# Optimization experiments

Hardware: AMD Instinct MI355X
Metric: run time of the kernel (lower is better)

Reference implementation:

```python
import jax, jax.numpy as jnp
import numpy as np

SQRT_2 = 1.414213
RT = 1.0  # Disk sets self.rt = 1.0
N_KPTS = 8192
M_KPTS = 8192
F_DIM = 256  # SuperPoint descriptor dim


def setup_inputs() -> dict:
    key = jax.random.key(0)
    k0, k1, k2, k3 = jax.random.split(key, 4)
    d0 = jax.random.normal(k0, (1, F_DIM, N_KPTS), dtype=jnp.float32)
    d1 = jax.random.normal(k1, (1, F_DIM, M_KPTS), dtype=jnp.float32)
    # distance_matrix assumes L2-normalized descriptors (normalize over F axis)
    d0 = d0 / jnp.linalg.norm(d0, axis=1, keepdims=True)
    d1 = d1 / jnp.linalg.norm(d1, axis=1, keepdims=True)
    kpts0 = jax.random.uniform(k2, (1, N_KPTS, 2), dtype=jnp.float32) * 480.0
    kpts1 = jax.random.uniform(k3, (1, M_KPTS, 2), dtype=jnp.float32) * 480.0
    return {"descriptors0": d0, "descriptors1": d1,
            "keypoints0": kpts0, "keypoints1": kpts1}


def _ratio_nn(dist):
    """Per-row nearest neighbor + Lowe ratio test. dist: [A, B].
    Returns (nn_idx [A] int32, pass_mask [A] bool)."""
    neg2, idx2 = jax.lax.top_k(-dist, 2)  # two smallest distances per row
    d1, d2 = -neg2[:, 0], -neg2[:, 1]
    return idx2[:, 0], (d1 / d2) < RT


def reference(descriptors0, descriptors1, keypoints0, keypoints1):
    fs0 = descriptors0[0].T  # [N, F]
    fs1 = descriptors1[0].T  # [M, F]
    # cosine -> L2-on-unit-sphere distance matrix, clamped as in the source
    dist = SQRT_2 * jnp.sqrt(jnp.clip(1.0 - fs0 @ fs1.T, 1e-6, None))  # [N, M]

    fwd_nn, fwd_ok = _ratio_nn(dist)    # [N]
    bck_nn, bck_ok = _ratio_nn(dist.T)  # [M]

    # mutual NN: (i, fwd_nn[i]) is kept iff the backward pass produced the
    # flipped pair (i, fwd_nn[i]) too -> same as counts==2 in the torch merge
    n = fs0.shape[0]
    mutual = fwd_ok & bck_ok[fwd_nn] & (bck_nn[fwd_nn] == jnp.arange(n))

    indices0 = jnp.where(mutual, fwd_nn, -1)[None, :].astype(jnp.int32)  # [1, N]
    mscores0 = jnp.where(indices0 > 0, 1, 0).astype(jnp.int32)           # [1, N]
    matches1 = jnp.full(keypoints1.shape[:-1], -1, dtype=jnp.int32)      # [1, M]
    mscores1 = jnp.zeros(keypoints1.shape[:-1], dtype=keypoints1.dtype)  # [1, M]
    return indices0, matches1, mscores0, mscores1
```

## Files before the change

kernel.cpp:

```cpp
#include <hip/hip_runtime.h>
#include <float.h>

#define NPTS 8192
#define MPTS 8192
#define FDIM 256

#define BM 128
#define BN 128
#define BK 32
#define TCT (MPTS / BN)
#define TRT (NPTS / BM)

typedef unsigned short ushort_t;
typedef unsigned int u32;
typedef __attribute__((ext_vector_type(8))) short short8;
typedef __attribute__((ext_vector_type(4))) float floatx4;

struct T2 { float s1, s2; int i1; };

__device__ __forceinline__ T2 t2_sent() { T2 a; a.s1 = -FLT_MAX; a.s2 = -FLT_MAX; a.i1 = 0; return a; }

__device__ __forceinline__ T2 t2_merge(T2 a, T2 b) {
    T2 r;
    r.s1 = fmaxf(a.s1, b.s1);
    r.i1 = (b.s1 > a.s1) ? b.i1 : a.i1;
    r.s2 = fmaxf(fminf(a.s1, b.s1), fmaxf(a.s2, b.s2));
    return r;
}
__device__ __forceinline__ T2 t2_make4(float v0, float v1, float v2, float v3,
                                       int i0, int i1_, int i2, int i3) {
    float lo01 = fminf(v0, v1), hi01 = fmaxf(v0, v1);
    float lo23 = fminf(v2, v3), hi23 = fmaxf(v2, v3);
    int a01 = (v1 > v0) ? i1_ : i0;
    int a23 = (v3 > v2) ? i3 : i2;
    T2 r;
    r.s1 = fmaxf(hi01, hi23);
    r.i1 = (hi23 > hi01) ? a23 : a01;
    r.s2 = fmaxf(fminf(hi01, hi23), fmaxf(lo01, lo23));
    return r;
}
__device__ __forceinline__ float4 t2_pack(T2 a) {
    return make_float4(a.s1, a.s2, __int_as_float(a.i1), 0.0f);
}
__device__ __forceinline__ T2 t2_unpack(float4 v) {
    T2 a; a.s1 = v.x; a.s2 = v.y; a.i1 = __float_as_int(v.z); return a;
}
__device__ __forceinline__ T2 t2_shfl_xor(T2 a, int m) {
    T2 r; r.s1 = __shfl_xor(a.s1, m); r.s2 = __shfl_xor(a.s2, m); r.i1 = __shfl_xor(a.i1, m);
    return r;
}

__device__ __forceinline__ float bf2f(ushort_t u) {
    union { u32 i; float f; } v; v.i = ((u32)u) << 16; return v.f;
}
__device__ __forceinline__ ushort_t f2bf_rtne(float x) {
    u32 u = __float_as_uint(x);
    u32 r = u + 0x7FFFu + ((u >> 16) & 1u);
    return (ushort_t)(r >> 16);
}

__global__ __launch_bounds__(256) void transpose_split(
    const float* __restrict__ s0, const float* __restrict__ s1,
    ushort_t* __restrict__ hi0, ushort_t* __restrict__ lo0,
    ushort_t* __restrict__ hi1, ushort_t* __restrict__ lo1)
{
    __shared__ ushort_t hiS[64][66];
    __shared__ ushort_t loS[64][66];
    const float* src = blockIdx.z ? s1 : s0;
    ushort_t* hiT = blockIdx.z ? hi1 : hi0;
    ushort_t* loT = blockIdx.z ? lo1 : lo0;
    const int t = threadIdx.x;
    const int n0 = blockIdx.x * 64, f0 = blockIdx.y * 64;

#pragma unroll
    for (int p = 0; p < 4; p++) {
        int fl = (t >> 4) + p * 16;
        int nl = (t & 15) * 4;
        float4 x = *(const float4*)&src[(size_t)(f0 + fl) * NPTS + n0 + nl];
        float xs[4] = {x.x, x.y, x.z, x.w};
#pragma unroll
        for (int e = 0; e < 4; e++) {
            ushort_t hb = f2bf_rtne(xs[e]);
            ushort_t lb = f2bf_rtne(xs[e] - bf2f(hb));
            hiS[nl + e][fl] = hb;
            loS[nl + e][fl] = lb;
        }
    }
    __syncthreads();
#pragma unroll
    for (int p = 0; p < 8; p++) {
        int nl = (t >> 5) + p * 8;
        int fp = (t & 31) * 2;
        u32 hw = (u32)hiS[nl][fp] | ((u32)hiS[nl][fp + 1] << 16);
        u32 lw = (u32)loS[nl][fp] | ((u32)loS[nl][fp + 1] << 16);
        size_t o = (size_t)(n0 + nl) * FDIM + f0 + fp;
        *(u32*)&hiT[o] = hw;
        *(u32*)&loT[o] = lw;
    }
}

#define GLDS(g, l) __builtin_amdgcn_global_load_lds( \
    (const __attribute__((address_space(1))) void*)(g), \
    (__attribute__((address_space(3))) void*)(l), 16, 0, 0)

#define STAGE(k0v, bufp) do { \
    _Pragma("unroll") for (int cc = 0; cc < 2; cc++) { \
        int _so = srcOff[cc] + (k0v); \
        char* _lb = (bufp) + ldsOff[cc]; \
        GLDS(bAh + _so, _lb); \
        GLDS(bBh + _so, _lb + 8192); \
        GLDS(bAl + _so, _lb + 16384); \
        GLDS(bBl + _so, _lb + 24576); \
    } \
} while (0)

#define READ_ALL(Pb) do { \
    _Pragma("unroll") for (int i = 0; i < 4; i++) { \
        ah[i] = *(const short8*)((Pb) + aoff[i]); \
        al[i] = *(const short8*)((Pb) + 16384 + aoff[i]); \
        bh[i] = *(const short8*)((Pb) + 8192 + boff[i]); \
        bl[i] = *(const short8*)((Pb) + 24576 + boff[i]); \
    } \
} while (0)

#define MFMA48 do { \
    _Pragma("unroll") for (int i = 0; i < 4; i++) \
    _Pragma("unroll") for (int j = 0; j < 4; j++) { \
        acc[i][j] = __builtin_amdgcn_mfma_f32_16x16x32_bf16(ah[i], bh[j], acc[i][j], 0, 0, 0); \
        acc[i][j] = __builtin_amdgcn_mfma_f32_16x16x32_bf16(ah[i], bl[j], acc[i][j], 0, 0, 0); \
        acc[i][j] = __builtin_amdgcn_mfma_f32_16x16x32_bf16(al[i], bh[j], acc[i][j], 0, 0, 0); \
    } \
} while (0)

#define KSTEP(ksv, Pb, Qb) do { \
    STAGE(((ksv) + 1) * BK, Qb); \
    asm volatile("s_waitcnt vmcnt(8)" ::: "memory"); \
    __builtin_amdgcn_s_barrier(); \
    READ_ALL(Pb); \
    asm volatile("s_waitcnt lgkmcnt(0)" ::: "memory"); \
    __builtin_amdgcn_sched_barrier(0); \
    MFMA48; \
    __builtin_amdgcn_sched_barrier(0); \
    __builtin_amdgcn_s_barrier(); \
} while (0)

__global__ __launch_bounds__(256, 2) void gemm_top2(
    const ushort_t* __restrict__ hiA, const ushort_t* __restrict__ loA,
    const ushort_t* __restrict__ hiB, const ushort_t* __restrict__ loB,
    float4* __restrict__ rowPart, float4* __restrict__ colPart)
{
    __shared__ char smem[65536];
    float* scrS1 = (float*)smem;
    float* scrS2 = (float*)(smem + 8448);
    int*   scrI  = (int*)(smem + 16896);
    float4* redC = (float4*)(smem + 25600);

    const int t = threadIdx.x;
    const int lane = t & 63, lc = lane & 15, q = lane >> 4;
    const int w = t >> 6, wx = w & 1, wy = w >> 1;
    const int ctile = blockIdx.x, rtile = blockIdx.y;
    const int n0 = rtile * BM, m0 = ctile * BN;

    floatx4 acc[4][4];
#pragma unroll
    for (int i = 0; i < 4; i++)
#pragma unroll
        for (int j = 0; j < 4; j++) acc[i][j] = (floatx4)0.0f;

    int srcOff[2], ldsOff[2];
#pragma unroll
    for (int cc = 0; cc < 2; cc++) {
        int L = cc * 256 + t;
        int row = L >> 2;
        int g = (L & 3) ^ ((L >> 3) & 3);
        srcOff[cc] = row * FDIM + g * 8;
        ldsOff[cc] = L * 16;
    }
    const ushort_t* bAh = hiA + (size_t)n0 * FDIM;
    const ushort_t* bAl = loA + (size_t)n0 * FDIM;
    const ushort_t* bBh = hiB + (size_t)m0 * FDIM;
    const ushort_t* bBl = loB + (size_t)m0 * FDIM;

    const int xa = (q ^ ((lc >> 1) & 3)) * 16;
    int aoff[4], boff[4];
#pragma unroll
    for (int i = 0; i < 4; i++) {
        aoff[i] = (wy * 64 + i * 16 + lc) * 64 + xa;
        boff[i] = (wx * 64 + i * 16 + lc) * 64 + xa;
    }

    short8 ah[4], al[4], bh[4], bl[4];

    char* buf0 = smem;
    char* buf1 = smem + 32768;
    STAGE(0, buf0);
#pragma unroll 1
    for (int kp = 0; kp < 3; kp++) {
        KSTEP(2 * kp, buf0, buf1);
        KSTEP(2 * kp + 1, buf1, buf0);
    }
    KSTEP(6, buf0, buf1);
    {
        asm volatile("s_waitcnt vmcnt(0)" ::: "memory");
        __builtin_amdgcn_s_barrier();
        READ_ALL(buf1);
        asm volatile("s_waitcnt lgkmcnt(0)" ::: "memory");
        __builtin_amdgcn_sched_barrier(0);
        MFMA48;
    }
    __syncthreads();

    T2 colT[4];
#pragma unroll
    for (int j = 0; j < 4; j++) colT[j] = t2_sent();
    T2 rowT[4][4];

    const int cb = m0 + wx * 64 + lc;
#pragma unroll
    for (int i = 0; i < 4; i++) {
#pragma unroll
        for (int r = 0; r < 4; r++)
            rowT[i][r] = t2_make4(acc[i][0][r], acc[i][1][r], acc[i][2][r], acc[i][3][r],
                                  cb, cb + 16, cb + 32, cb + 48);
        const int rb = n0 + wy * 64 + i * 16 + q * 4;
#pragma unroll
        for (int j = 0; j < 4; j++)
            colT[j] = t2_merge(colT[j],
                t2_make4(acc[i][j][0], acc[i][j][1], acc[i][j][2], acc[i][j][3],
                         rb, rb + 1, rb + 2, rb + 3));
    }

#pragma unroll
    for (int j = 0; j < 4; j++) {
        colT[j] = t2_merge(colT[j], t2_shfl_xor(colT[j], 16));
        colT[j] = t2_merge(colT[j], t2_shfl_xor(colT[j], 32));
        if (q == 0) redC[(wx * 64 + j * 16 + lc) * 2 + wy] = t2_pack(colT[j]);
    }

#pragma unroll
    for (int round = 0; round < 2; round++) {
        __syncthreads();
        if (wy == round) {
#pragma unroll
            for (int i = 0; i < 4; i++)
#pragma unroll
                for (int r = 0; r < 4; r++) {
                    int row = i * 16 + q * 4 + r;
                    int col = (lc << 1) | wx;
                    int slot = row * 33 + ((col + row + 9 * q) & 31);
                    scrS1[slot] = rowT[i][r].s1;
                    scrS2[slot] = rowT[i][r].s2;
                    scrI[slot]  = rowT[i][r].i1;
                }
        }
        __syncthreads();
        {
            int row = t >> 2, chunk = t & 3;
            T2 a = t2_sent();
#pragma unroll
            for (int s = 0; s < 8; s++) {
                int slot = row * 33 + ((chunk << 3) | s);
                T2 b; b.s1 = scrS1[slot]; b.s2 = scrS2[slot]; b.i1 = scrI[slot];
                a = t2_merge(a, b);
            }
            a = t2_merge(a, t2_shfl_xor(a, 1));
            a = t2_merge(a, t2_shfl_xor(a, 2));
            if (chunk == 0)
                rowPart[(size_t)ctile * NPTS + n0 + round * 64 + row] = t2_pack(a);
        }
    }

    __syncthreads();
    if (t < 128) {
        T2 m = t2_unpack(redC[t * 2 + 0]);
        m = t2_merge(m, t2_unpack(redC[t * 2 + 1]));
        colPart[(size_t)rtile * MPTS + m0 + t] = t2_pack(m);
    }
}

__global__ __launch_bounds__(256) void reduce_final(
    const float4* __restrict__ rowPart, const float4* __restrict__ colPart,
    float* __restrict__ out)
{
    __shared__ float4 sh[4][64];
    __shared__ int shFwd[64];
    __shared__ int shOk[64];
    const int t = threadIdx.x, nl = t & 63, sub = t >> 6;
    const int n = blockIdx.x * 64 + nl;

    T2 a = t2_sent();
#pragma unroll
    for (int k = 0; k < 16; k++)
        a = t2_merge(a, t2_unpack(rowPart[(size_t)(sub * 16 + k) * NPTS + n]));
    sh[sub][nl] = t2_pack(a);
    __syncthreads();
    if (t < 64) {
        T2 r = t2_unpack(sh[0][t]);
        r = t2_merge(r, t2_unpack(sh[1][t]));
        r = t2_merge(r, t2_unpack(sh[2][t]));
        r = t2_merge(r, t2_unpack(sh[3][t]));
        float c1 = fmaxf(1.0f - r.s1, 1e-6f), c2 = fmaxf(1.0f - r.s2, 1e-6f);
        float d1 = 1.414213f * sqrtf(c1), d2 = 1.414213f * sqrtf(c2);
        shFwd[t] = r.i1;
        shOk[t]  = ((d1 / d2) < 1.0f) ? 1 : 0;
    }
    __syncthreads();
    const int fw = shFwd[nl];
    T2 c = t2_sent();
#pragma unroll
    for (int k = 0; k < 16; k++)
        c = t2_merge(c, t2_unpack(colPart[(size_t)(sub * 16 + k) * MPTS + fw]));
    sh[sub][nl] = t2_pack(c);
    __syncthreads();
    if (t < 64) {
        T2 r = t2_unpack(sh[0][t]);
        r = t2_merge(r, t2_unpack(sh[1][t]));
        r = t2_merge(r, t2_unpack(sh[2][t]));
        r = t2_merge(r, t2_unpack(sh[3][t]));
        float c1 = fmaxf(1.0f - r.s1, 1e-6f), c2 = fmaxf(1.0f - r.s2, 1e-6f);
        float d1 = 1.414213f * sqrtf(c1), d2 = 1.414213f * sqrtf(c2);
        bool bok = (d1 / d2) < 1.0f;
        int nn = blockIdx.x * 64 + t;
        bool mutual = (shOk[t] != 0) && bok && (r.i1 == nn);
        int idx0 = mutual ? shFwd[t] : -1;
        out[nn]             = (float)idx0;
        out[NPTS + nn]      = -1.0f;
        out[2 * NPTS + nn]  = (idx0 > 0) ? 1.0f : 0.0f;
        out[3 * NPTS + nn]  = 0.0f;
    }
}

extern "C" void kernel_launch(void* const* d_in, const int* in_sizes, int n_in,
                              void* d_out, int out_size, void* d_ws, size_t ws_size,
                              hipStream_t stream)
{
    const float* d0 = (const float*)d_in[0];
    const float* d1 = (const float*)d_in[1];

    char* ws = (char*)d_ws;
    const size_t matB = (size_t)NPTS * FDIM * sizeof(ushort_t);
    ushort_t* hiA = (ushort_t*)(ws);
    ushort_t* loA = (ushort_t*)(ws + matB);
    ushort_t* hiB = (ushort_t*)(ws + 2 * matB);
    ushort_t* loB = (ushort_t*)(ws + 3 * matB);
    char* p = ws + 4 * matB;
    const size_t rowBytes = (size_t)TCT * NPTS * sizeof(float4);
    float4* rowPart = (float4*)p;
    float4* colPart = (float4*)(p + rowBytes);

    dim3 gt(NPTS / 64, FDIM / 64, 2);
    transpose_split<<<gt, 256, 0, stream>>>(d0, d1, hiA, loA, hiB, loB);

    dim3 g1(TCT, TRT);
    gemm_top2<<<g1, 256, 0, stream>>>(hiA, loA, hiB, loB, rowPart, colPart);
    reduce_final<<<NPTS / 64, 256, 0, stream>>>(rowPart, colPart, (float*)d_out);
}
```

Measured before the change: 191.9 us.

## Single-buffer LDS staging and split B fragments to raise occupancy to 3 blocks

Replaces the double-buffered global_load_lds pipeline with a single 32KB LDS buffer and barrier-synchronized stage/compute steps. B fragments are loaded in two halves to cut register pressure, and launch bounds are raised to 3 blocks per CU. The aim is to hide latency through occupancy rather than through software prefetch, but within each block global loads no longer overlap MFMA work.

```diff
diff --git a/kernel.cpp b/kernel.cpp
--- a/kernel.cpp
+++ b/kernel.cpp
@@ -103,10 +103,10 @@
     (const __attribute__((address_space(1))) void*)(g), \
     (__attribute__((address_space(3))) void*)(l), 16, 0, 0)
 
-#define STAGE(k0v, bufp) do { \
+#define STAGE(k0v) do { \
     _Pragma("unroll") for (int cc = 0; cc < 2; cc++) { \
         int _so = srcOff[cc] + (k0v); \
-        char* _lb = (bufp) + ldsOff[cc]; \
+        char* _lb = smem + ldsOff[cc]; \
         GLDS(bAh + _so, _lb); \
         GLDS(bBh + _so, _lb + 8192); \
         GLDS(bAl + _so, _lb + 16384); \
@@ -114,42 +114,35 @@
     } \
 } while (0)
 
-#define READ_ALL(Pb) do { \
+#define READ_A() do { \
     _Pragma("unroll") for (int i = 0; i < 4; i++) { \
-        ah[i] = *(const short8*)((Pb) + aoff[i]); \
-        al[i] = *(const short8*)((Pb) + 16384 + aoff[i]); \
-        bh[i] = *(const short8*)((Pb) + 8192 + boff[i]); \
-        bl[i] = *(const short8*)((Pb) + 24576 + boff[i]); \
+        ah[i] = *(const short8*)(smem + aoff[i]); \
+        al[i] = *(const short8*)(smem + 16384 + aoff[i]); \
     } \
 } while (0)
 
-#define MFMA48 do { \
-    _Pragma("unroll") for (int i = 0; i < 4; i++) \
-    _Pragma("unroll") for (int j = 0; j < 4; j++) { \
-        acc[i][j] = __builtin_amdgcn_mfma_f32_16x16x32_bf16(ah[i], bh[j], acc[i][j], 0, 0, 0); \
-        acc[i][j] = __builtin_amdgcn_mfma_f32_16x16x32_bf16(ah[i], bl[j], acc[i][j], 0, 0, 0); \
-        acc[i][j] = __builtin_amdgcn_mfma_f32_16x16x32_bf16(al[i], bh[j], acc[i][j], 0, 0, 0); \
+#define READ_B2(J0) do { \
+    _Pragma("unroll") for (int jj = 0; jj < 2; jj++) { \
+        bh[jj] = *(const short8*)(smem + 8192 + boff[(J0) + jj]); \
+        bl[jj] = *(const short8*)(smem + 24576 + boff[(J0) + jj]); \
     } \
 } while (0)
 
-#define KSTEP(ksv, Pb, Qb) do { \
-    STAGE(((ksv) + 1) * BK, Qb); \
-    asm volatile("s_waitcnt vmcnt(8)" ::: "memory"); \
-    __builtin_amdgcn_s_barrier(); \
-    READ_ALL(Pb); \
-    asm volatile("s_waitcnt lgkmcnt(0)" ::: "memory"); \
-    __builtin_amdgcn_sched_barrier(0); \
-    MFMA48; \
-    __builtin_amdgcn_sched_barrier(0); \
-    __builtin_amdgcn_s_barrier(); \
+#define MFMA24(J0) do { \
+    _Pragma("unroll") for (int i = 0; i < 4; i++) \
+    _Pragma("unroll") for (int jj = 0; jj < 2; jj++) { \
+        acc[i][(J0) + jj] = __builtin_amdgcn_mfma_f32_16x16x32_bf16(ah[i], bh[jj], acc[i][(J0) + jj], 0, 0, 0); \
+        acc[i][(J0) + jj] = __builtin_amdgcn_mfma_f32_16x16x32_bf16(ah[i], bl[jj], acc[i][(J0) + jj], 0, 0, 0); \
+        acc[i][(J0) + jj] = __builtin_amdgcn_mfma_f32_16x16x32_bf16(al[i], bh[jj], acc[i][(J0) + jj], 0, 0, 0); \
+    } \
 } while (0)
 
-__global__ __launch_bounds__(256, 2) void gemm_top2(
+__global__ __launch_bounds__(256, 3) void gemm_top2(
     const ushort_t* __restrict__ hiA, const ushort_t* __restrict__ loA,
     const ushort_t* __restrict__ hiB, const ushort_t* __restrict__ loB,
     float4* __restrict__ rowPart, float4* __restrict__ colPart)
 {
-    __shared__ char smem[65536];
+    __shared__ char smem[32768];
     float* scrS1 = (float*)smem;
     float* scrS2 = (float*)(smem + 8448);
     int*   scrI  = (int*)(smem + 16896);
@@ -189,24 +182,19 @@
         boff[i] = (wx * 64 + i * 16 + lc) * 64 + xa;
     }
 
-    short8 ah[4], al[4], bh[4], bl[4];
-
-    char* buf0 = smem;
-    char* buf1 = smem + 32768;
-    STAGE(0, buf0);
+    short8 ah[4], al[4], bh[2], bl[2];
+
 #pragma unroll 1
-    for (int kp = 0; kp < 3; kp++) {
-        KSTEP(2 * kp, buf0, buf1);
-        KSTEP(2 * kp + 1, buf1, buf0);
-    }
-    KSTEP(6, buf0, buf1);
-    {
-        asm volatile("s_waitcnt vmcnt(0)" ::: "memory");
-        __builtin_amdgcn_s_barrier();
-        READ_ALL(buf1);
-        asm volatile("s_waitcnt lgkmcnt(0)" ::: "memory");
+    for (int ks = 0; ks < 8; ks++) {
+        if (ks) __syncthreads();
+        STAGE(ks * BK);
+        __syncthreads();
+        READ_A();
+        READ_B2(0);
+        MFMA24(0);
         __builtin_amdgcn_sched_barrier(0);
-        MFMA48;
+        READ_B2(2);
+        MFMA24(2);
     }
     __syncthreads();
 
```

Measured after the change: 185.2 us (median of 2 runs). -3.5%, faster.
